# Kernel optimization log

Hardware: AMD Instinct MI355X
Metric: run time of the kernel (lower is better)

Reference implementation:

```python
import jax, jax.numpy as jnp
import numpy as np

D_IN = 1024
D_OUT = 1024
NUM_HEADS = 16
HEAD_DIM = D_OUT // NUM_HEADS


def setup_inputs() -> dict:
    key = jax.random.key(0)
    ks = jax.random.split(key, 6)
    s = 0.02
    return {
        "x": jax.random.normal(ks[0], (4, 2048, D_IN), dtype=jnp.float32),
        "Wq": jax.random.normal(ks[1], (D_IN, D_OUT), dtype=jnp.float32) * s,
        "Wk": jax.random.normal(ks[2], (D_IN, D_OUT), dtype=jnp.float32) * s,
        "Wv": jax.random.normal(ks[3], (D_IN, D_OUT), dtype=jnp.float32) * s,
        "Wo": jax.random.normal(ks[4], (D_OUT, D_OUT), dtype=jnp.float32) * s,
        "bo": jax.random.normal(ks[5], (D_OUT,), dtype=jnp.float32) * s,
    }


def reference(x, Wq, Wk, Wv, Wo, bo):
    B, T, _ = x.shape
    H, Dh = NUM_HEADS, HEAD_DIM
    # projections -> [B, H, T, Dh]
    q = (x @ Wq).reshape(B, T, H, Dh).transpose(0, 2, 1, 3)
    k = (x @ Wk).reshape(B, T, H, Dh).transpose(0, 2, 1, 3)
    v = (x @ Wv).reshape(B, T, H, Dh).transpose(0, 2, 1, 3)
    # scores [B, H, T, T]
    scores = jnp.einsum('bhqd,bhkd->bhqk', q, k)
    causal = jnp.triu(jnp.ones((T, T), dtype=bool), k=1)
    scores = jnp.where(causal, -jnp.inf, scores)
    attn = jax.nn.softmax(scores / jnp.sqrt(jnp.float32(Dh)), axis=-1)
    # dropout=0.0 -> identity
    ctx = jnp.einsum('bhqk,bhkd->bhqd', attn, v)
    ctx = ctx.transpose(0, 2, 1, 3).reshape(B, T, H * Dh)
    return ctx @ Wo + bo
```

## Files before the change

### kernel.cpp

```cpp
#include <hip/hip_runtime.h>
#include <hip/hip_bf16.h>
#include <stdint.h>

#define TSEQ 2048
#define DMODEL 1024

typedef __attribute__((ext_vector_type(8))) short bf16x8;
typedef __attribute__((ext_vector_type(4))) float f32x4;
typedef __attribute__((ext_vector_type(16))) float f32x16;

union Frag { bf16x8 v; uint4 q; };

__device__ __forceinline__ uint16_t f2bfu(float f) {
  uint32_t u = __builtin_bit_cast(uint32_t, f);
  u += 0x7fffu + ((u >> 16) & 1u);
  return (uint16_t)(u >> 16);
}

__device__ __forceinline__ uint32_t pk2bf(float a, float b) {
  return ((uint32_t)f2bfu(b) << 16) | f2bfu(a);
}

__device__ __forceinline__ uint32_t cvtpk(float a, float b) {
  uint32_t r;
  asm("v_cvt_pk_bf16_f32 %0, %1, %2" : "=v"(r) : "v"(a), "v"(b));
  return r;
}

__device__ __forceinline__ float fexp2(float x) {
#if __has_builtin(__builtin_amdgcn_exp2f)
  return __builtin_amdgcn_exp2f(x);
#else
  return exp2f(x);
#endif
}

__device__ __forceinline__ void gload_lds16(const void* g, void* l) {
  __builtin_amdgcn_global_load_lds(
      (const __attribute__((address_space(1))) void*)g,
      (__attribute__((address_space(3))) void*)l, 16, 0, 0);
}


__global__ __launch_bounds__(256) void cvt_x_kernel(const float* __restrict__ x,
                                                    uint16_t* __restrict__ xb, int n4) {
  int i = blockIdx.x * 256 + threadIdx.x;
  if (i >= n4) return;
  float4 v = ((const float4*)x)[i];
  ushort4 o;
  o.x = f2bfu(v.x); o.y = f2bfu(v.y); o.z = f2bfu(v.z); o.w = f2bfu(v.w);
  ((ushort4*)xb)[i] = o;
}

__global__ __launch_bounds__(256) void cvt_w_kernel(const float* __restrict__ Wq,
    const float* __restrict__ Wk, const float* __restrict__ Wv, const float* __restrict__ Wo,
    uint16_t* __restrict__ Wqkvt, uint16_t* __restrict__ Wot) {
  const float* src = (blockIdx.z == 0) ? Wq : (blockIdx.z == 1) ? Wk
                   : (blockIdx.z == 2) ? Wv : Wo;
  uint16_t* dst = (blockIdx.z < 3) ? (Wqkvt + (size_t)blockIdx.z * DMODEL * DMODEL) : Wot;
  const float wscale = (blockIdx.z == 0) ? 0.125f * 1.4426950408889634f : 1.0f;
  __shared__ float tile[32][33];
  const int x0 = blockIdx.x * 32, y0 = blockIdx.y * 32;
  for (int ii = 0; ii < 4; ii++) {
    int i = threadIdx.y + ii * 8;
    tile[i][threadIdx.x] = src[(size_t)(y0 + i) * DMODEL + x0 + threadIdx.x];
  }
  __syncthreads();
  for (int ii = 0; ii < 4; ii++) {
    int i = threadIdx.y + ii * 8;
    dst[(size_t)(x0 + i) * DMODEL + y0 + threadIdx.x] = f2bfu(tile[threadIdx.x][i] * wscale);
  }
}

__device__ __forceinline__ void stage256(const char* Gb, int kb, char* ldsT, int tid) {
#pragma unroll
  for (int r = 0; r < 4; ++r) {
    const int u = tid + r * 512;
    const int row = u >> 3;
    const int sc = ((u & 7) * 16) ^ ((row & 7) << 4);
    gload_lds16(Gb + (size_t)row * 2048 + kb + sc, ldsT + u * 16);
  }
}


__device__ __forceinline__ void gemm256sq_core(const char* Ab, const char* Bb,
                                               char* lds,
                                               f32x4 (&acc)[8][4]) {
  const int tid = threadIdx.x;
  const int lane = tid & 63;
  const int w = tid >> 6;
  const int lr = lane & 15, lg = lane >> 4;
  const int wmb = (w >> 2) * 128;
  const int wnb = (w & 3) * 64;
  char* const A0 = lds;
  char* const A1 = lds + 32768;
  char* const B0 = lds + 65536;
  char* const B1 = lds + 98304;

#pragma unroll
  for (int i = 0; i < 8; i++)
#pragma unroll
    for (int j = 0; j < 4; j++) acc[i][j] = (f32x4){0.f, 0.f, 0.f, 0.f};

  stage256(Ab, 0, A0, tid);
  stage256(Bb, 0, B0, tid);
  for (int t = 0; t < 16; ++t) {
    const char* At = (t & 1) ? A1 : A0;
    const char* Bt = (t & 1) ? B1 : B0;
    char* nA = (t & 1) ? A0 : A1;
    char* nB = (t & 1) ? B0 : B1;
    if (t + 1 < 16) {
      stage256(Ab, (t + 1) * 128, nA, tid);
      asm volatile("s_waitcnt vmcnt(4)" ::: "memory");
    } else {
      asm volatile("s_waitcnt vmcnt(0)" ::: "memory");
    }
    __builtin_amdgcn_s_barrier();
    __builtin_amdgcn_sched_barrier(0);

    Frag bf0[4], bf1[4];
#pragma unroll
    for (int ni = 0; ni < 4; ni++) {
      const int row = wnb + ni * 16 + lr;
      const int swz = (row & 7) << 4;
      bf0[ni].q = *(const uint4*)(Bt + row * 128 + ((lg * 16) ^ swz));
      bf1[ni].q = *(const uint4*)(Bt + row * 128 + ((64 + lg * 16) ^ swz));
    }
#pragma unroll
    for (int ph = 0; ph < 4; ph++) {
      Frag a0[2], a1[2];
#pragma unroll
      for (int i = 0; i < 2; i++) {
        const int row = wmb + (2 * ph + i) * 16 + lr;
        const int swz = (row & 7) << 4;
        a0[i].q = *(const uint4*)(At + row * 128 + ((lg * 16) ^ swz));
        a1[i].q = *(const uint4*)(At + row * 128 + ((64 + lg * 16) ^ swz));
      }
      __builtin_amdgcn_s_setprio(1);
#pragma unroll
      for (int i = 0; i < 2; i++) {
        const int mi = 2 * ph + i;
#pragma unroll
        for (int ni = 0; ni < 4; ni++) {
          acc[mi][ni] = __builtin_amdgcn_mfma_f32_16x16x32_bf16(a0[i].v, bf0[ni].v,
                                                                acc[mi][ni], 0, 0, 0);
          acc[mi][ni] = __builtin_amdgcn_mfma_f32_16x16x32_bf16(a1[i].v, bf1[ni].v,
                                                                acc[mi][ni], 0, 0, 0);
        }
      }
      __builtin_amdgcn_s_setprio(0);
      if (ph == 0 && t + 1 < 16) stage256(Bb, (t + 1) * 128, nB, tid);
    }
    __builtin_amdgcn_s_barrier();
  }
}


__global__ __launch_bounds__(512, 2) void gemm_qk_kernel(const uint16_t* __restrict__ Xb,
    const uint16_t* __restrict__ Wt, uint16_t* __restrict__ Qo,
    uint16_t* __restrict__ Ko) {
  __shared__ __align__(16) char lds[131072];
  const int m0 = (blockIdx.x & 31) * 256;
  const int n0 = (blockIdx.x >> 5) * 256;
  f32x4 acc[8][4];
  gemm256sq_core((const char*)Xb + (size_t)m0 * 2048, (const char*)Wt + (size_t)n0 * 2048,
                 lds, acc);

  const int tid = threadIdx.x, w = tid >> 6, lane = tid & 63;
  const int lr = lane & 15, lg = lane >> 4;
  const int wmb = (w >> 2) * 128, wnb = (w & 3) * 64;
#pragma unroll
  for (int mi = 0; mi < 8; mi++)
#pragma unroll
    for (int ni = 0; ni < 4; ni++) {
      const int col = n0 + wnb + ni * 16 + lr;
      const int p = col >> 10, c = col & 1023, h = c >> 6, d = c & 63;
#pragma unroll
      for (int r = 0; r < 4; r++) {
        const int row = m0 + wmb + mi * 16 + 4 * lg + r;
        const int bb = row >> 11, t = row & 2047;
        const int bh = bb * 16 + h;
        const uint16_t val = f2bfu(acc[mi][ni][r]);
        if (p == 0) Qo[((size_t)bh * TSEQ + t) * 64 + d] = val;
        else        Ko[((size_t)bh * TSEQ + t) * 64 + d] = val;
      }
    }
}


__device__ __forceinline__ void g8_stage_p1(const char* Ab, int kb, char* ldsA, int tid) {
#pragma unroll
  for (int r = 0; r < 3; ++r) {
    const int u = tid + r * 512;
    const int row = u >> 3;
    const int sc = ((u & 7) * 16) ^ ((row & 7) << 4);
    gload_lds16(Ab + (size_t)row * 2048 + kb + sc, ldsA + u * 16);
  }
}

__device__ __forceinline__ void g8_stage_p2(const char* Ab, const char* Bb, int kb,
                                            char* ldsA, char* ldsB, int tid) {
  {
    const int u = tid + 3 * 512;
    const int row = u >> 3;
    const int sc = ((u & 7) * 16) ^ ((row & 7) << 4);
    gload_lds16(Ab + (size_t)row * 2048 + kb + sc, ldsA + u * 16);
  }
#pragma unroll
  for (int r = 0; r < 2; ++r) {
    const int u = tid + r * 512;
    const int row = u >> 3;
    const int sc = ((u & 7) * 16) ^ ((row & 7) << 4);
    gload_lds16(Bb + (size_t)row * 2048 + kb + sc, ldsB + u * 16);
  }
}

__device__ __forceinline__ void gemm256x128_core(const char* Ab, const char* Bb,
                                                 char* lds,
                                                 f32x4 (&acc)[4][4]) {
  const int tid = threadIdx.x;
  const int lane = tid & 63;
  const int w = tid >> 6;
  const int lr = lane & 15, lg = lane >> 4;
  const int wmb = (w >> 1) * 64;
  const int wnb = (w & 1) * 64;
  char* const A0 = lds;
  char* const A1 = lds + 32768;
  char* const B0 = lds + 65536;
  char* const B1 = lds + 81920;

#pragma unroll
  for (int i = 0; i < 4; i++)
#pragma unroll
    for (int j = 0; j < 4; j++) acc[i][j] = (f32x4){0.f, 0.f, 0.f, 0.f};

  g8_stage_p1(Ab, 0, A0, tid);
  g8_stage_p2(Ab, Bb, 0, A0, B0, tid);
  for (int t = 0; t < 16; ++t) {
    const char* At = (t & 1) ? A1 : A0;
    const char* Bt = (t & 1) ? B1 : B0;
    char* nA = (t & 1) ? A0 : A1;
    char* nB = (t & 1) ? B0 : B1;
    if (t + 1 < 16) {
      g8_stage_p1(Ab, (t + 1) * 128, nA, tid);
      asm volatile("s_waitcnt vmcnt(3)" ::: "memory");
    } else {
      asm volatile("s_waitcnt vmcnt(0)" ::: "memory");
    }
    __builtin_amdgcn_s_barrier();
    __builtin_amdgcn_sched_barrier(0);

    Frag bf0[4], bf1[4];
#pragma unroll
    for (int ni = 0; ni < 4; ni++) {
      const int row = wnb + ni * 16 + lr;
      const int swz = (row & 7) << 4;
      bf0[ni].q = *(const uint4*)(Bt + row * 128 + ((lg * 16) ^ swz));
      bf1[ni].q = *(const uint4*)(Bt + row * 128 + ((64 + lg * 16) ^ swz));
    }
    Frag pa0[2], pa1[2];
#pragma unroll
    for (int mi = 0; mi < 2; mi++) {
      const int row = wmb + mi * 16 + lr;
      const int swz = (row & 7) << 4;
      pa0[mi].q = *(const uint4*)(At + row * 128 + ((lg * 16) ^ swz));
      pa1[mi].q = *(const uint4*)(At + row * 128 + ((64 + lg * 16) ^ swz));
    }
    __builtin_amdgcn_s_setprio(1);
#pragma unroll
    for (int mi = 0; mi < 2; mi++)
#pragma unroll
      for (int ni = 0; ni < 4; ni++) {
        acc[mi][ni] = __builtin_amdgcn_mfma_f32_16x16x32_bf16(pa0[mi].v, bf0[ni].v,
                                                              acc[mi][ni], 0, 0, 0);
        acc[mi][ni] = __builtin_amdgcn_mfma_f32_16x16x32_bf16(pa1[mi].v, bf1[ni].v,
                                                              acc[mi][ni], 0, 0, 0);
      }
    __builtin_amdgcn_s_setprio(0);

    if (t + 1 < 16) g8_stage_p2(Ab, Bb, (t + 1) * 128, nA, nB, tid);
#pragma unroll
    for (int mi = 2; mi < 4; mi++) {
      const int row = wmb + mi * 16 + lr;
      const int swz = (row & 7) << 4;
      Frag qa0, qa1;
      qa0.q = *(const uint4*)(At + row * 128 + ((lg * 16) ^ swz));
      qa1.q = *(const uint4*)(At + row * 128 + ((64 + lg * 16) ^ swz));
      __builtin_amdgcn_s_setprio(1);
#pragma unroll
      for (int ni = 0; ni < 4; ni++) {
        acc[mi][ni] = __builtin_amdgcn_mfma_f32_16x16x32_bf16(qa0.v, bf0[ni].v,
                                                              acc[mi][ni], 0, 0, 0);
        acc[mi][ni] = __builtin_amdgcn_mfma_f32_16x16x32_bf16(qa1.v, bf1[ni].v,
                                                              acc[mi][ni], 0, 0, 0);
      }
      __builtin_amdgcn_s_setprio(0);
    }
    __builtin_amdgcn_s_barrier();
  }
}


__global__ __launch_bounds__(512, 2) void gemm_v_kernel(const uint16_t* __restrict__ Xb,
    const uint16_t* __restrict__ Wtv, uint16_t* __restrict__ Vt) {
  __shared__ __align__(16) char lds[98304];
  const int m0 = (blockIdx.x & 31) * 256;
  const int n0 = (blockIdx.x >> 5) * 128;
  f32x4 acc[4][4];
  gemm256x128_core((const char*)Xb + (size_t)m0 * 2048, (const char*)Wtv + (size_t)n0 * 2048,
                   lds, acc);

  const int tid = threadIdx.x, w = tid >> 6, lane = tid & 63;
  const int lr = lane & 15, lg = lane >> 4;
  const int wmb = (w >> 1) * 64;

  char* vr = lds + (w & 1) * 33792;
#pragma unroll
  for (int mi = 0; mi < 4; mi++)
#pragma unroll
    for (int ni = 0; ni < 4; ni++) {
      const int d = ni * 16 + lr;
      const int tl = wmb + mi * 16 + 4 * lg;
      uint2 pr;
      pr.x = cvtpk(acc[mi][ni][0], acc[mi][ni][1]);
      pr.y = cvtpk(acc[mi][ni][2], acc[mi][ni][3]);
      *(uint2*)(vr + d * 528 + tl * 2) = pr;
    }
  __syncthreads();
  const int bb = m0 >> 11, t0 = m0 & 2047;
  const int h0 = n0 >> 6;
#pragma unroll
  for (int j = 0; j < 8; j++) {
    const int linear = (tid + j * 512) * 16;
    const int rg = linear >> 15;
    const int rem = linear & 32767;
    const int d = rem >> 9;
    const int toff = rem & 511;
    const uint4 val = *(const uint4*)(lds + rg * 33792 + d * 528 + toff);
    const int bh = bb * 16 + h0 + rg;
    *(uint4*)((char*)Vt + ((size_t)(bh * 64 + d) * TSEQ + t0) * 2 + toff) = val;
  }
}


__device__ __forceinline__ void stage_kv(const char* Kb, const char* Vb, int kv0,
                                         char* kdst, char* vdst, int tid) {
  const int w1024 = (tid >> 6) * 1024;
#pragma unroll
  for (int i = 0; i < 2; i++) {
    const int o = i * 4096 + tid * 16;
    const int row = o >> 7;
    const int scol = (o & 127) ^ ((row & 7) << 4);
    gload_lds16(Kb + (size_t)(kv0 + row) * 128 + scol, kdst + i * 4096 + w1024);
    gload_lds16(Vb + (size_t)row * 4096 + kv0 * 2 + scol, vdst + i * 4096 + w1024);
  }
}

__global__ __launch_bounds__(256, 3) void attn_kernel(const uint16_t* __restrict__ Qw,
    const uint16_t* __restrict__ Kw, const uint16_t* __restrict__ Vtw,
    uint16_t* __restrict__ Ctx) {
  const int bid = blockIdx.x;
  const int qt = 15 - (bid >> 6);
  const int bh = bid & 63;
  const int tid = threadIdx.x;
  const int w = tid >> 6, lane = tid & 63;
  const int lq = lane & 31;
  const int hi = lane >> 5;
  const int wq0 = qt * 128 + w * 32;

  const char* Qb = (const char*)Qw + (size_t)bh * TSEQ * 128;
  const char* Kb = (const char*)Kw + (size_t)bh * TSEQ * 128;
  const char* Vb = (const char*)Vtw + (size_t)bh * 64 * 4096;

  __shared__ __align__(16) char kbuf[2][8192];
  __shared__ __align__(16) char vbuf[2][8192];

  Frag qa[4];
#pragma unroll
  for (int kc = 0; kc < 4; kc++)
    qa[kc].q = *(const uint4*)(Qb + (size_t)(wq0 + lq) * 128 + kc * 32 + hi * 16);

  f32x16 o0 = 0.f, o1 = 0.f;
  float mrun = -1e30f, lrun = 0.f;

  const int nt = 2 * qt + 2;
  stage_kv(Kb, Vb, 0, kbuf[0], vbuf[0], tid);
  int cur = 0;
  for (int t = 0; t < nt; ++t) {
    const int kv0 = t * 64;
    if (t + 1 < nt) {
      stage_kv(Kb, Vb, kv0 + 64, kbuf[cur ^ 1], vbuf[cur ^ 1], tid);
      asm volatile("s_waitcnt vmcnt(4)" ::: "memory");
    } else {
      asm volatile("s_waitcnt vmcnt(0)" ::: "memory");
    }
    __builtin_amdgcn_s_barrier();
    __builtin_amdgcn_sched_barrier(0);

    if (kv0 <= wq0 + 31) {
      const char* Kt = kbuf[cur];
      const char* Vt = vbuf[cur];
      f32x16 s[2];
#pragma unroll
      for (int kvh = 0; kvh < 2; kvh++) {
        f32x16 acc = 0.f;
#pragma unroll
        for (int kc = 0; kc < 4; kc++) {
          const int row = kvh * 32 + lq;
          Frag kf;
          kf.q = *(const uint4*)(Kt + row * 128 + ((kc * 32 + hi * 16) ^ ((row & 7) << 4)));
          acc = __builtin_amdgcn_mfma_f32_32x32x16_bf16(kf.v, qa[kc].v, acc, 0, 0, 0);
        }
        s[kvh] = acc;
      }
      if (kv0 + 63 > wq0) {
        const int q_abs = wq0 + lq;
#pragma unroll
        for (int kvh = 0; kvh < 2; kvh++)
#pragma unroll
          for (int r = 0; r < 16; r++) {
            const int kv_abs = kv0 + kvh * 32 + (r & 3) + 8 * (r >> 2) + 4 * hi;
            if (kv_abs > q_abs) s[kvh][r] = -1e30f;
          }
      }
      float t8[8];
#pragma unroll
      for (int i = 0; i < 8; i++)
        t8[i] = fmaxf(fmaxf(s[0][2 * i], s[0][2 * i + 1]),
                      fmaxf(s[1][2 * i], s[1][2 * i + 1]));
      float t4a = fmaxf(t8[0], t8[1]), t4b = fmaxf(t8[2], t8[3]);
      float t4c = fmaxf(t8[4], t8[5]), t4d = fmaxf(t8[6], t8[7]);
      float mt = fmaxf(fmaxf(t4a, t4b), fmaxf(t4c, t4d));
      mt = fmaxf(mt, __shfl_xor(mt, 32));
      if (!__all(mt - mrun <= 8.0f)) {
        const float mnew = fmaxf(mrun, mt);
        const float corr = fexp2(mrun - mnew);
        mrun = mnew;
        lrun *= corr;
        o0 *= corr;
        o1 *= corr;
      }
#pragma unroll
      for (int kvh = 0; kvh < 2; kvh++)
#pragma unroll
        for (int r = 0; r < 16; r++) s[kvh][r] = fexp2(s[kvh][r] - mrun);
      float ps = 0.f;
#pragma unroll
      for (int kvh = 0; kvh < 2; kvh++)
#pragma unroll
        for (int r = 0; r < 16; r++) ps += s[kvh][r];
      ps += __shfl_xor(ps, 32);
      lrun += ps;
      uint32_t pk[2][8];
#pragma unroll
      for (int kvh = 0; kvh < 2; kvh++)
#pragma unroll
        for (int j = 0; j < 8; j++)
          pk[kvh][j] = cvtpk(s[kvh][2 * j], s[kvh][2 * j + 1]);
#pragma unroll
      for (int c16 = 0; c16 < 4; c16++) {
        const int kvh = c16 >> 1, cl = c16 & 1;
        const uint32_t s0 = (uint32_t)__shfl_xor((int)pk[kvh][4 * cl + 0], 32);
        const uint32_t s1 = (uint32_t)__shfl_xor((int)pk[kvh][4 * cl + 1], 32);
        const uint32_t s2 = (uint32_t)__shfl_xor((int)pk[kvh][4 * cl + 2], 32);
        const uint32_t s3 = (uint32_t)__shfl_xor((int)pk[kvh][4 * cl + 3], 32);
        Frag pb;
        pb.q.x = hi ? s2 : pk[kvh][4 * cl + 0];
        pb.q.y = hi ? s3 : pk[kvh][4 * cl + 1];
        pb.q.z = hi ? pk[kvh][4 * cl + 2] : s0;
        pb.q.w = hi ? pk[kvh][4 * cl + 3] : s1;
#pragma unroll
        for (int dblk = 0; dblk < 2; dblk++) {
          const int row = dblk * 32 + lq;
          Frag vf;
          vf.q = *(const uint4*)(Vt + row * 128 + ((c16 * 32 + hi * 16) ^ ((row & 7) << 4)));
          if (dblk == 0)
            o0 = __builtin_amdgcn_mfma_f32_32x32x16_bf16(vf.v, pb.v, o0, 0, 0, 0);
          else
            o1 = __builtin_amdgcn_mfma_f32_32x32x16_bf16(vf.v, pb.v, o1, 0, 0, 0);
        }
      }
    }
    __builtin_amdgcn_s_barrier();
    cur ^= 1;
  }

  const int bb = bh >> 4, hh = bh & 15;
  const float inv = 1.0f / lrun;
  const int q_abs = wq0 + lq;
  uint16_t* crow = Ctx + ((size_t)bb * TSEQ + q_abs) * DMODEL + hh * 64;
#pragma unroll
  for (int dblk = 0; dblk < 2; dblk++)
#pragma unroll
    for (int g = 0; g < 4; g++) {
      const float a0 = (dblk ? o1[4 * g + 0] : o0[4 * g + 0]) * inv;
      const float a1 = (dblk ? o1[4 * g + 1] : o0[4 * g + 1]) * inv;
      const float a2 = (dblk ? o1[4 * g + 2] : o0[4 * g + 2]) * inv;
      const float a3 = (dblk ? o1[4 * g + 3] : o0[4 * g + 3]) * inv;
      uint2 st;
      st.x = cvtpk(a0, a1);
      st.y = cvtpk(a2, a3);
      *(uint2*)(crow + dblk * 32 + 8 * g + 4 * hi) = st;
    }
}


__global__ __launch_bounds__(512, 2) void gemm_out_kernel(const uint16_t* __restrict__ Cb,
    const uint16_t* __restrict__ Wot, const float* __restrict__ bo,
    float* __restrict__ out) {
  __shared__ __align__(16) char lds[98304];
  const int m0 = (blockIdx.x & 31) * 256;
  const int n0 = (blockIdx.x >> 5) * 128;
  f32x4 acc[4][4];
  gemm256x128_core((const char*)Cb + (size_t)m0 * 2048, (const char*)Wot + (size_t)n0 * 2048,
                   lds, acc);

  const int tid = threadIdx.x, w = tid >> 6, lane = tid & 63;
  const int lr = lane & 15, lg = lane >> 4;
  const int wmb = (w >> 1) * 64, wnb = (w & 1) * 64;
#pragma unroll
  for (int mi = 0; mi < 4; mi++)
#pragma unroll
    for (int ni = 0; ni < 4; ni++) {
      const int col = n0 + wnb + ni * 16 + lr;
      const float bias = bo[col];
#pragma unroll
      for (int r = 0; r < 4; r++) {
        const int row = m0 + wmb + mi * 16 + 4 * lg + r;
        out[(size_t)row * DMODEL + col] = acc[mi][ni][r] + bias;
      }
    }
}


extern "C" void kernel_launch(void* const* d_in, const int* in_sizes, int n_in,
                              void* d_out, int out_size, void* d_ws, size_t ws_size,
                              hipStream_t stream) {
  const float* x  = (const float*)d_in[0];
  const float* Wq = (const float*)d_in[1];
  const float* Wk = (const float*)d_in[2];
  const float* Wv = (const float*)d_in[3];
  const float* Wo = (const float*)d_in[4];
  const float* bo = (const float*)d_in[5];
  float* out = (float*)d_out;

  char* ws = (char*)d_ws;
  uint16_t* Xb    = (uint16_t*)(ws);
  uint16_t* Ctx   = (uint16_t*)(ws);
  uint16_t* Wqkvt = (uint16_t*)(ws + (16u << 20));
  uint16_t* Wot   = (uint16_t*)(ws + (22u << 20));
  uint16_t* Qw    = (uint16_t*)(ws + (24u << 20));
  uint16_t* Kw    = (uint16_t*)(ws + (40u << 20));
  uint16_t* Vtw   = (uint16_t*)(ws + (56u << 20));
  (void)ws_size; (void)in_sizes; (void)n_in; (void)out_size;

  cvt_x_kernel<<<8192, 256, 0, stream>>>(x, Xb, 2097152);
  cvt_w_kernel<<<dim3(32, 32, 4), dim3(32, 8), 0, stream>>>(Wq, Wk, Wv, Wo, Wqkvt, Wot);
  gemm_qk_kernel<<<256, 512, 0, stream>>>(Xb, Wqkvt, Qw, Kw);
  gemm_v_kernel<<<256, 512, 0, stream>>>(Xb, Wqkvt + (size_t)2048 * 1024, Vtw);
  attn_kernel<<<1024, 256, 0, stream>>>(Qw, Kw, Vtw, Ctx);
  gemm_out_kernel<<<256, 512, 0, stream>>>(Ctx, Wot, bo, out);
}
```

Before: 169.2 us.

## Use permlane32_swap for P transpose, raise attention occupancy, rebalance causal tile order

The P-fragment half-wave exchange now uses the permlane32_swap builtin instead of four shfl_xor calls plus selects, with the old path kept as a fallback. Attention launch bounds go from 3 to 4 blocks per CU, which tightens the register budget. Causal q-tiles are handed out in a zigzag order (heavy, mid, mid, light) per 256-block round to balance load across CUs. The tighter register cap could cause spills.

```diff
diff --git a/kernel.cpp b/kernel.cpp
--- a/kernel.cpp
+++ b/kernel.cpp
@@ -8,6 +8,7 @@
 typedef __attribute__((ext_vector_type(8))) short bf16x8;
 typedef __attribute__((ext_vector_type(4))) float f32x4;
 typedef __attribute__((ext_vector_type(16))) float f32x16;
+typedef __attribute__((ext_vector_type(2))) int int2v;
 
 union Frag { bf16x8 v; uint4 q; };
 
@@ -25,6 +26,22 @@
   uint32_t r;
   asm("v_cvt_pk_bf16_f32 %0, %1, %2" : "=v"(r) : "v"(a), "v"(b));
   return r;
+}
+
+__device__ __forceinline__ void plane32swap(uint32_t& a, uint32_t& b) {
+#if __has_builtin(__builtin_amdgcn_permlane32_swap)
+  int2v r = __builtin_amdgcn_permlane32_swap((int)a, (int)b, false, false);
+  a = (uint32_t)r[0];
+  b = (uint32_t)r[1];
+#else
+  const uint32_t sa = (uint32_t)__shfl_xor((int)a, 32);
+  const uint32_t sb = (uint32_t)__shfl_xor((int)b, 32);
+  const bool hi = (threadIdx.x & 63) >= 32;
+  const uint32_t na = hi ? sb : a;
+  const uint32_t nb = hi ? b : sa;
+  a = na;
+  b = nb;
+#endif
 }
 
 __device__ __forceinline__ float fexp2(float x) {
@@ -356,12 +373,19 @@
   }
 }
 
-__global__ __launch_bounds__(256, 3) void attn_kernel(const uint16_t* __restrict__ Qw,
+__global__ __launch_bounds__(256, 4) void attn_kernel(const uint16_t* __restrict__ Qw,
     const uint16_t* __restrict__ Kw, const uint16_t* __restrict__ Vtw,
     uint16_t* __restrict__ Ctx) {
   const int bid = blockIdx.x;
-  const int qt = 15 - (bid >> 6);
-  const int bh = bid & 63;
+  const int c = bid & 255;
+  const int rd = bid >> 8;
+  const int g = c >> 6;
+  int qt;
+  if (rd == 0)      qt = 15 - g;
+  else if (rd == 1) qt = 8 + g;
+  else if (rd == 2) qt = 7 - g;
+  else              qt = g;
+  const int bh = c & 63;
   const int tid = threadIdx.x;
   const int w = tid >> 6, lane = tid & 63;
   const int lq = lane & 31;
@@ -460,15 +484,15 @@
 #pragma unroll
       for (int c16 = 0; c16 < 4; c16++) {
         const int kvh = c16 >> 1, cl = c16 & 1;
-        const uint32_t s0 = (uint32_t)__shfl_xor((int)pk[kvh][4 * cl + 0], 32);
-        const uint32_t s1 = (uint32_t)__shfl_xor((int)pk[kvh][4 * cl + 1], 32);
-        const uint32_t s2 = (uint32_t)__shfl_xor((int)pk[kvh][4 * cl + 2], 32);
-        const uint32_t s3 = (uint32_t)__shfl_xor((int)pk[kvh][4 * cl + 3], 32);
+        uint32_t x0 = pk[kvh][4 * cl + 0], y0 = pk[kvh][4 * cl + 2];
+        uint32_t x1 = pk[kvh][4 * cl + 1], y1 = pk[kvh][4 * cl + 3];
+        plane32swap(x0, y0);
+        plane32swap(x1, y1);
         Frag pb;
-        pb.q.x = hi ? s2 : pk[kvh][4 * cl + 0];
-        pb.q.y = hi ? s3 : pk[kvh][4 * cl + 1];
-        pb.q.z = hi ? pk[kvh][4 * cl + 2] : s0;
-        pb.q.w = hi ? pk[kvh][4 * cl + 3] : s1;
+        pb.q.x = x0;
+        pb.q.y = x1;
+        pb.q.z = y0;
+        pb.q.w = y1;
 #pragma unroll
         for (int dblk = 0; dblk < 2; dblk++) {
           const int row = dblk * 32 + lq;
@@ -492,15 +516,15 @@
 #pragma unroll
   for (int dblk = 0; dblk < 2; dblk++)
 #pragma unroll
-    for (int g = 0; g < 4; g++) {
-      const float a0 = (dblk ? o1[4 * g + 0] : o0[4 * g + 0]) * inv;
-      const float a1 = (dblk ? o1[4 * g + 1] : o0[4 * g + 1]) * inv;
-      const float a2 = (dblk ? o1[4 * g + 2] : o0[4 * g + 2]) * inv;
-      const float a3 = (dblk ? o1[4 * g + 3] : o0[4 * g + 3]) * inv;
+    for (int g2 = 0; g2 < 4; g2++) {
+      const float a0 = (dblk ? o1[4 * g2 + 0] : o0[4 * g2 + 0]) * inv;
+      const float a1 = (dblk ? o1[4 * g2 + 1] : o0[4 * g2 + 1]) * inv;
+      const float a2 = (dblk ? o1[4 * g2 + 2] : o0[4 * g2 + 2]) * inv;
+      const float a3 = (dblk ? o1[4 * g2 + 3] : o0[4 * g2 + 3]) * inv;
       uint2 st;
       st.x = cvtpk(a0, a1);
       st.y = cvtpk(a2, a3);
-      *(uint2*)(crow + dblk * 32 + 8 * g + 4 * hi) = st;
+      *(uint2*)(crow + dblk * 32 + 8 * g2 + 4 * hi) = st;
     }
 }
 
```

After: 161.0 us. 1.05x faster.
